# Performance work log

Measured on AMD Instinct MI355X. Metric: run time of the kernel, lower is better.

The kernel has to match this reference:

```python
import jax, jax.numpy as jnp
import numpy as np

D_MODEL = 512
NUM_HEADS = 8
HEAD_DIM = D_MODEL // NUM_HEADS
MAX_REL = 2


def setup_inputs() -> dict:
    key = jax.random.key(0)
    ks = jax.random.split(key, 12)
    B, S = 2, 4096
    std = 1.0 / np.sqrt(D_MODEL)
    inp = {
        'q': jax.random.normal(ks[0], (B, S, D_MODEL), jnp.float32),
        'k': jax.random.normal(ks[1], (B, S, D_MODEL), jnp.float32),
        'v': jax.random.normal(ks[2], (B, S, D_MODEL), jnp.float32),
        'Wq': jax.random.normal(ks[3], (D_MODEL, D_MODEL), jnp.float32) * std,
        'bq': jnp.zeros((D_MODEL,), jnp.float32),
        'Wk': jax.random.normal(ks[4], (D_MODEL, D_MODEL), jnp.float32) * std,
        'bk': jnp.zeros((D_MODEL,), jnp.float32),
        'Wv': jax.random.normal(ks[5], (D_MODEL, D_MODEL), jnp.float32) * std,
        'bv': jnp.zeros((D_MODEL,), jnp.float32),
        'Wo': jax.random.normal(ks[6], (D_MODEL, D_MODEL), jnp.float32) * std,
        'bo': jnp.zeros((D_MODEL,), jnp.float32),
        'rel_pos': jax.random.normal(ks[7], (NUM_HEADS, 2 * MAX_REL + 1), jnp.float32),
    }
    return inp


def _rel_bias(rel_pos, seq_len):
    pos = jnp.arange(seq_len)
    rel = pos[None, :] - pos[:, None]              # [S,S]
    idx = jnp.clip(rel, -MAX_REL, MAX_REL) + MAX_REL
    return rel_pos[:, idx]                         # [H,S,S]


def reference(q, k, v, Wq, bq, Wk, bk, Wv, bv, Wo, bo, rel_pos):
    B, S, D = q.shape
    H, Hd = NUM_HEADS, HEAD_DIM
    # torch Linear: x @ W.T + b
    Q = (q @ Wq.T + bq).reshape(B, S, H, Hd).transpose(0, 2, 1, 3)  # [B,H,S,Hd]
    K = (k @ Wk.T + bk).reshape(B, S, H, Hd).transpose(0, 2, 1, 3)
    V = (v @ Wv.T + bv).reshape(B, S, H, Hd).transpose(0, 2, 1, 3)
    scores = jnp.einsum('bhqd,bhkd->bhqk', Q, K) / jnp.sqrt(jnp.float32(Hd))
    scores = scores + _rel_bias(rel_pos, S)[None]                  # [B,H,S,S]
    probs = jax.nn.softmax(scores, axis=-1)
    attn = jnp.einsum('bhqk,bhkd->bhqd', probs, V)                 # [B,H,S,Hd]
    attn = attn.transpose(0, 2, 1, 3).reshape(B, S, D)
    return attn @ Wo.T + bo
```

## Files before the change

### kernel.cpp

```cpp
#include <hip/hip_runtime.h>

typedef __bf16 bf16_t;
typedef __bf16 bf16x2 __attribute__((ext_vector_type(2)));
typedef __bf16 bf16x4 __attribute__((ext_vector_type(4)));
typedef __bf16 bf16x8 __attribute__((ext_vector_type(8)));
typedef float f32x4 __attribute__((ext_vector_type(4)));
typedef unsigned int u32x4 __attribute__((ext_vector_type(4)));

#define MFMA16(a, b, c) __builtin_amdgcn_mfma_f32_16x16x32_bf16(a, b, c, 0, 0, 0)
#define LOG2E 1.4426950408889634f
#define SHIFT 16.0f

#define GLL(g, l)                                                      \
  __builtin_amdgcn_global_load_lds(                                    \
      (const __attribute__((address_space(1))) void*)(g),              \
      (__attribute__((address_space(3))) void*)(l), 16, 0, 0)

#define WAIT_BARRIER_V0() asm volatile("s_waitcnt vmcnt(0)\n\ts_barrier" ::: "memory")
#define WAIT_BARRIER_V6() asm volatile("s_waitcnt vmcnt(6)\n\ts_barrier" ::: "memory")

static constexpr int NB = 2;
static constexpr int SEQ = 4096;
static constexpr int DM = 512;
static constexpr int NH = 8;
static constexpr int HD = 64;
static constexpr int M_ROWS = NB * SEQ;

__global__ __launch_bounds__(256) void cvt_w_kernel(
    const float* __restrict__ w0, const float* __restrict__ w1,
    const float* __restrict__ w2, const float* __restrict__ w3,
    bf16_t* __restrict__ out) {
  const float* src = (blockIdx.y == 0) ? w0 : (blockIdx.y == 1) ? w1
                   : (blockIdx.y == 2) ? w2 : w3;
  int i = (blockIdx.x * 256 + threadIdx.x) * 4;
  float4 v = *(const float4*)(src + i);
  bf16_t* o = out + blockIdx.y * (DM * DM) + i;
  o[0] = (bf16_t)v.x; o[1] = (bf16_t)v.y; o[2] = (bf16_t)v.z; o[3] = (bf16_t)v.w;
}

__global__ __launch_bounds__(256) void cvt_x_kernel(
    const float* __restrict__ q, const float* __restrict__ k,
    const float* __restrict__ v, bf16_t* __restrict__ out) {
  const float* src = (blockIdx.y == 0) ? q : (blockIdx.y == 1) ? k : v;
  bf16_t* dst = out + (size_t)blockIdx.y * (M_ROWS * DM);
  int i = (blockIdx.x * 256 + threadIdx.x) * 8;
  float4 a = *(const float4*)(src + i);
  float4 b = *(const float4*)(src + i + 4);
  bf16x8 o;
  o[0] = (bf16_t)a.x; o[1] = (bf16_t)a.y; o[2] = (bf16_t)a.z; o[3] = (bf16_t)a.w;
  o[4] = (bf16_t)b.x; o[5] = (bf16_t)b.y; o[6] = (bf16_t)b.z; o[7] = (bf16_t)b.w;
  *(bf16x8*)(dst + i) = o;
}

__device__ __forceinline__ void gemm_body64(
    const bf16_t* __restrict__ X, const bf16_t* __restrict__ Wm,
    const float* __restrict__ bias, void* __restrict__ Out,
    int omode, float scale) {
  __shared__ bf16_t Asm[3][64 * 64];
  __shared__ bf16_t Bsm[3][128 * 64];

  const int tid = threadIdx.x;
  const int w = tid >> 6;
  const int lane = tid & 63;
  const int quad = lane >> 4, l15 = lane & 15;
  const int l8 = lane >> 3;
  const int swcol = ((lane & 7) ^ l8) * 8;
  const int m0 = blockIdx.x * 64;
  const int n0 = blockIdx.y * 128;
  const int moff = (w & 1) * 32;
  const int noff = (w >> 1) * 64;

  f32x4 acc[2][4];
#pragma unroll
  for (int mb = 0; mb < 2; mb++)
#pragma unroll
    for (int nb = 0; nb < 4; nb++) { acc[mb][nb][0] = 0.f; acc[mb][nb][1] = 0.f; acc[mb][nb][2] = 0.f; acc[mb][nb][3] = 0.f; }

  auto stage = [&](int ks, int bufi) {
    const int k0 = ks * 64;
#pragma unroll
    for (int j = 0; j < 4; j++) {
      const int row = j * 32 + w * 8 + l8;
      GLL(Wm + (size_t)(n0 + row) * DM + k0 + swcol, &Bsm[bufi][(j * 256 + w * 64) * 8]);
    }
#pragma unroll
    for (int j = 0; j < 2; j++) {
      const int row = j * 32 + w * 8 + l8;
      GLL(X + (size_t)(m0 + row) * DM + k0 + swcol, &Asm[bufi][(j * 256 + w * 64) * 8]);
    }
  };

  stage(0, 0);
  stage(1, 1);

  for (int ks = 0; ks < 8; ks++) {
    WAIT_BARRIER_V6();
    const int tn = (ks + 2 < 8) ? ks + 2 : 7;
    stage(tn, (ks + 2) % 3);
    const int p = ks % 3;

#pragma unroll
    for (int kd = 0; kd < 2; kd++) {
      const int fch = (((kd << 2) + quad) ^ (l15 & 7)) << 3;
      bf16x8 bfr[4];
#pragma unroll
      for (int nb = 0; nb < 4; nb++)
        bfr[nb] = *(const bf16x8*)&Bsm[p][(noff + nb * 16 + l15) * 64 + fch];
#pragma unroll
      for (int mb = 0; mb < 2; mb++) {
        bf16x8 a = *(const bf16x8*)&Asm[p][(moff + mb * 16 + l15) * 64 + fch];
#pragma unroll
        for (int nb = 0; nb < 4; nb++) acc[mb][nb] = MFMA16(a, bfr[nb], acc[mb][nb]);
      }
    }
  }

#pragma unroll
  for (int nb = 0; nb < 4; nb++) {
    const int n = n0 + noff + nb * 16 + l15;
    const float bn = bias[n];
    const int h = n >> 6, dd = n & 63;
#pragma unroll
    for (int mb = 0; mb < 2; mb++) {
      const int mbase = m0 + moff + mb * 16 + quad * 4;
      const int bb = mbase >> 12, s = mbase & 4095;
      if (omode == 0) {
#pragma unroll
        for (int r = 0; r < 4; r++) {
          const float val = (acc[mb][nb][r] + bn) * scale;
          ((bf16_t*)Out)[(size_t)((bb * NH + h) * SEQ + s + r) * HD + dd] = (bf16_t)val;
        }
      } else if (omode == 1) {
        bf16x4 pk;
#pragma unroll
        for (int r = 0; r < 4; r++) pk[r] = (bf16_t)(acc[mb][nb][r] + bn);
        *(bf16x4*)&((bf16_t*)Out)[(((size_t)(bb * NH + h) * HD + dd) << 12) + s] = pk;
      } else {
#pragma unroll
        for (int r = 0; r < 4; r++)
          ((float*)Out)[(size_t)(mbase + r) * DM + n] = acc[mb][nb][r] + bn;
      }
    }
  }
}

__global__ __launch_bounds__(256, 2) void qkv_kernel(
    const bf16_t* __restrict__ Xall, const bf16_t* __restrict__ Wall,
    const float* __restrict__ bq, const float* __restrict__ bk,
    const float* __restrict__ bv, bf16_t* __restrict__ Qb,
    bf16_t* __restrict__ Kb, bf16_t* __restrict__ Vb, float qscale) {
  const int z = blockIdx.z;
  const bf16_t* X = Xall + (size_t)z * (M_ROWS * DM);
  const float* bias = (z == 0) ? bq : (z == 1) ? bk : bv;
  bf16_t* Out = (z == 0) ? Qb : (z == 1) ? Kb : Vb;
  gemm_body64(X, Wall + (size_t)z * DM * DM, bias, Out,
              (z == 2) ? 1 : 0, (z == 0) ? qscale : 1.0f);
}

__global__ __launch_bounds__(256, 2) void oproj_kernel(
    const bf16_t* __restrict__ X, const bf16_t* __restrict__ Wm,
    const float* __restrict__ bias, float* __restrict__ Out) {
  gemm_body64(X, Wm, bias, Out, 2, 1.0f);
}

__global__ __launch_bounds__(256, 2) void attn_kernel(
    const bf16_t* __restrict__ Qb, const bf16_t* __restrict__ Kb,
    const bf16_t* __restrict__ Vb, const float* __restrict__ rel_pos,
    bf16_t* __restrict__ attn_out) {
  __shared__ bf16_t Kt[4][64 * 64];
  __shared__ bf16_t Vt[4][64 * 64];

  const int tid = threadIdx.x;
  const int w = tid >> 6;
  const int lane = tid & 63;
  const int quad = lane >> 4, l15 = lane & 15;
  const int wq = w >> 1, wk = w & 1;

  const int lin = blockIdx.x;
  const int glob = (lin & 7) * 64 + (lin >> 3);
  const int bh = glob >> 5;
  const int qb = glob & 31;
  const int b = bh >> 3, h = bh & 7;
  const int qlo = qb * 128 + wq * 64;

  const float rb0 = rel_pos[h * 5 + 0] * LOG2E;
  const float rb1 = rel_pos[h * 5 + 1] * LOG2E;
  const float rb2 = rel_pos[h * 5 + 2] * LOG2E;
  const float rb3 = rel_pos[h * 5 + 3] * LOG2E;
  const float rb4 = rel_pos[h * 5 + 4] * LOG2E;

  bf16x8 qf[4][2];
#pragma unroll
  for (int mb = 0; mb < 4; mb++)
#pragma unroll
    for (int kd = 0; kd < 2; kd++)
      qf[mb][kd] = *(const bf16x8*)(Qb + (size_t)(bh * SEQ + qlo + mb * 16 + l15) * HD + kd * 32 + 8 * quad);

  f32x4 o[4][4];
#pragma unroll
  for (int mb = 0; mb < 4; mb++)
#pragma unroll
    for (int db = 0; db < 4; db++) { o[mb][db][0] = 0.f; o[mb][db][1] = 0.f; o[mb][db][2] = 0.f; o[mb][db][3] = 0.f; }
  f32x4 l4[4];
#pragma unroll
  for (int mb = 0; mb < 4; mb++) { l4[mb][0] = 0.f; l4[mb][1] = 0.f; l4[mb][2] = 0.f; l4[mb][3] = 0.f; }

  bf16x8 ones;
#pragma unroll
  for (int i = 0; i < 8; i++) ones[i] = (bf16_t)1.0f;

  const int srow = (w << 4) + (lane >> 3);
  const int scol = (((lane & 7) ^ (lane >> 3)) << 3);
  const bf16_t* kg0 = Kb + ((size_t)(bh * SEQ + srow) << 6) + scol;
  const bf16_t* vg0 = Vb + (((size_t)(bh * HD + srow)) << 12) + scol;
  const int ldst = (w << 10);

  const int sw = l15 & 7;
  const int kfo0 = (l15 << 6) + ((quad ^ sw) << 3);
  const int kfo1 = (l15 << 6) + (((quad + 4) ^ sw) << 3);
  const int vfo = (l15 << 6) + ((((wk << 2) + quad) ^ sw) << 3);
  const int wk2 = wk << 1;

  auto stage = [&](int t, int bufi) {
    GLL(kg0 + ((size_t)t << 12), &Kt[bufi][ldst]);
    GLL(kg0 + ((size_t)t << 12) + (8 << 6), &Kt[bufi][ldst + 512]);
    GLL(vg0 + (t << 6), &Vt[bufi][ldst]);
    GLL(vg0 + (t << 6) + (8 << 12), &Vt[bufi][ldst + 512]);
  };

  auto qk_tile = [&](int tq, f32x4 (&s)[4][2]) {
    const int klo = tq * 64 + wk * 32;
    float cini;
    if (klo >= qlo + 65)        cini = rb4 - SHIFT;
    else if (klo <= qlo - 33)   cini = rb0 - SHIFT;
    else                        cini = -SHIFT;
#pragma unroll
    for (int mb = 0; mb < 4; mb++)
#pragma unroll
      for (int kb = 0; kb < 2; kb++) { s[mb][kb][0] = cini; s[mb][kb][1] = cini; s[mb][kb][2] = cini; s[mb][kb][3] = cini; }
    const int pq = tq & 3;
    __builtin_amdgcn_s_setprio(1);
#pragma unroll
    for (int kb = 0; kb < 2; kb++) {
      bf16x8 kA0 = *(const bf16x8*)&Kt[pq][kfo0 + ((wk2 + kb) << 10)];
      bf16x8 kA1 = *(const bf16x8*)&Kt[pq][kfo1 + ((wk2 + kb) << 10)];
      s[0][kb] = MFMA16(kA0, qf[0][0], s[0][kb]);
      s[0][kb] = MFMA16(kA1, qf[0][1], s[0][kb]);
      s[1][kb] = MFMA16(kA0, qf[1][0], s[1][kb]);
      s[1][kb] = MFMA16(kA1, qf[1][1], s[1][kb]);
      s[2][kb] = MFMA16(kA0, qf[2][0], s[2][kb]);
      s[2][kb] = MFMA16(kA1, qf[2][1], s[2][kb]);
      s[3][kb] = MFMA16(kA0, qf[3][0], s[3][kb]);
      s[3][kb] = MFMA16(kA1, qf[3][1], s[3][kb]);
    }
    __builtin_amdgcn_s_setprio(0);
  };

  auto sm_pv = [&](int t, f32x4 (&s)[4][2]) {
    const int klo = t * 64 + wk * 32;
    const bool nearband = !(klo >= qlo + 65) && !(klo <= qlo - 33);
    if (nearband) {
#pragma unroll
      for (int mb = 0; mb < 4; mb++) {
        const int qg = qlo + mb * 16 + l15;
#pragma unroll
        for (int kb = 0; kb < 2; kb++)
#pragma unroll
          for (int r = 0; r < 4; r++) {
            int dl = klo + kb * 16 + quad * 4 + r - qg;
            float bias = dl <= -2 ? rb0
                       : (dl >= 2 ? rb4
                       : (dl == -1 ? rb1 : (dl == 0 ? rb2 : rb3)));
            s[mb][kb][r] += bias;
          }
      }
    }

    bf16x8 pf[4];
#pragma unroll
    for (int mb = 0; mb < 4; mb++) {
      unsigned int u[2][2];
#pragma unroll
      for (int kb = 0; kb < 2; kb++) {
        bf16x2 p0, p1;
        p0[0] = (bf16_t)__builtin_amdgcn_exp2f(s[mb][kb][0]);
        p0[1] = (bf16_t)__builtin_amdgcn_exp2f(s[mb][kb][1]);
        p1[0] = (bf16_t)__builtin_amdgcn_exp2f(s[mb][kb][2]);
        p1[1] = (bf16_t)__builtin_amdgcn_exp2f(s[mb][kb][3]);
        u[kb][0] = __builtin_bit_cast(unsigned int, p0);
        u[kb][1] = __builtin_bit_cast(unsigned int, p1);
      }
      unsigned int a0 = u[0][0], b0 = u[1][0];
      unsigned int a1 = u[0][1], b1 = u[1][1];
      asm("v_permlane32_swap_b32 %0, %1" : "+v"(a0), "+v"(b0));
      asm("v_permlane32_swap_b32 %0, %1" : "+v"(a1), "+v"(b1));
      asm("v_permlane16_swap_b32 %0, %1" : "+v"(a0), "+v"(b0));
      asm("v_permlane16_swap_b32 %0, %1" : "+v"(a1), "+v"(b1));
      u32x4 pk; pk[0] = a0; pk[1] = a1; pk[2] = b0; pk[3] = b1;
      pf[mb] = __builtin_bit_cast(bf16x8, pk);
    }

    const int p = t & 3;
    __builtin_amdgcn_s_setprio(1);
    l4[0] = MFMA16(ones, pf[0], l4[0]);
    l4[1] = MFMA16(ones, pf[1], l4[1]);
    l4[2] = MFMA16(ones, pf[2], l4[2]);
    l4[3] = MFMA16(ones, pf[3], l4[3]);
#pragma unroll
    for (int db = 0; db < 4; db++) {
      bf16x8 vA = *(const bf16x8*)&Vt[p][vfo + (db << 10)];
      o[0][db] = MFMA16(vA, pf[0], o[0][db]);
      o[1][db] = MFMA16(vA, pf[1], o[1][db]);
      o[2][db] = MFMA16(vA, pf[2], o[2][db]);
      o[3][db] = MFMA16(vA, pf[3], o[3][db]);
    }
    __builtin_amdgcn_s_setprio(0);
  };

  stage(0, 0);
  stage(1, 1);

  f32x4 sA[4][2], sB[4][2];

  for (int j = 0; j < 32; j++) {
    const int e = 2 * j, o2 = 2 * j + 1;
    WAIT_BARRIER_V0();
    const int ta = (e + 2 < 64) ? e + 2 : 63;
    const int tb = (o2 + 2 < 64) ? o2 + 2 : 63;
    stage(ta, (e + 2) & 3);
    stage(tb, (o2 + 2) & 3);
    qk_tile(e, sA);
    qk_tile(o2, sB);
    sm_pv(e, sA);
    sm_pv(o2, sB);
  }

  asm volatile("s_waitcnt vmcnt(0)" ::: "memory");
  __syncthreads();
  float* Ored = (float*)&Kt[0][0];
  float* lred = (float*)&Vt[0][0];
  if (wk) {
#pragma unroll
    for (int mb = 0; mb < 4; mb++) {
      lred[(wq << 6) + (mb << 4) + l15] = l4[mb][0];
#pragma unroll
      for (int db = 0; db < 4; db++) {
        const int ch = ((db << 2) | quad) ^ sw;
        *(f32x4*)&Ored[(wq << 12) + ((mb * 16 + l15) << 6) + (ch << 2)] = o[mb][db];
      }
    }
  }
  __syncthreads();
  if (!wk) {
#pragma unroll
    for (int mb = 0; mb < 4; mb++) {
      float lsum = l4[mb][0] + lred[(wq << 6) + (mb << 4) + l15];
      const float inv = 1.0f / lsum;
      const int qg = qlo + mb * 16 + l15;
#pragma unroll
      for (int db = 0; db < 4; db++) {
        const int ch = ((db << 2) | quad) ^ sw;
        const f32x4 part = *(const f32x4*)&Ored[(wq << 12) + ((mb * 16 + l15) << 6) + (ch << 2)];
        bf16x4 pk;
#pragma unroll
        for (int r = 0; r < 4; r++) pk[r] = (bf16_t)((o[mb][db][r] + part[r]) * inv);
        *(bf16x4*)(attn_out + (size_t)(b * SEQ + qg) * DM + h * HD + db * 16 + quad * 4) = pk;
      }
    }
  }
}

extern "C" void kernel_launch(void* const* d_in, const int* in_sizes, int n_in,
                              void* d_out, int out_size, void* d_ws, size_t ws_size,
                              hipStream_t stream) {
  const float* q   = (const float*)d_in[0];
  const float* k   = (const float*)d_in[1];
  const float* v   = (const float*)d_in[2];
  const float* Wq  = (const float*)d_in[3];
  const float* bq  = (const float*)d_in[4];
  const float* Wk  = (const float*)d_in[5];
  const float* bk  = (const float*)d_in[6];
  const float* Wv  = (const float*)d_in[7];
  const float* bv  = (const float*)d_in[8];
  const float* Wo  = (const float*)d_in[9];
  const float* bo  = (const float*)d_in[10];
  const float* rel = (const float*)d_in[11];

  char* ws = (char*)d_ws;
  bf16_t* Wbf  = (bf16_t*)ws;
  bf16_t* Xb   = (bf16_t*)(ws + (size_t)(2  << 20));
  bf16_t* Qbuf = (bf16_t*)(ws + (size_t)(26 << 20));
  bf16_t* Kbuf = (bf16_t*)(ws + (size_t)(34 << 20));
  bf16_t* Vbuf = (bf16_t*)(ws + (size_t)(42 << 20));
  bf16_t* Abuf = (bf16_t*)(ws + (size_t)(2  << 20));

  cvt_w_kernel<<<dim3(256, 4), 256, 0, stream>>>(Wq, Wk, Wv, Wo, Wbf);
  cvt_x_kernel<<<dim3(2048, 3), 256, 0, stream>>>(q, k, v, Xb);

  const float qscale = LOG2E / 8.0f;
  qkv_kernel<<<dim3(128, 4, 3), 256, 0, stream>>>(
      Xb, Wbf, bq, bk, bv, Qbuf, Kbuf, Vbuf, qscale);

  attn_kernel<<<512, 256, 0, stream>>>(Qbuf, Kbuf, Vbuf, rel, Abuf);

  oproj_kernel<<<dim3(128, 4), 256, 0, stream>>>(Abuf, Wbf + 3 * DM * DM, bo, (float*)d_out);
}
```

Baseline: 227.2 us.

## Halve attention query tile and K/V buffering to raise occupancy

The attention kernel now gives each block 64 queries instead of 128 and each wave 32 query rows instead of 64, and launches 1024 blocks. It cuts the K/V LDS ring from 4 stages to 2, drops the two-tile software pipelining in favour of a simple one-tile-per-iteration loop, and raises launch_bounds to 4 blocks per CU. The goal is more resident waves to hide latency, at the cost of loading each K/V tile for half as many queries (double the K/V traffic) and less prefetch depth. The near-band threshold is tightened to match the smaller query span.

```diff
diff --git a/kernel.cpp b/kernel.cpp
--- a/kernel.cpp
+++ b/kernel.cpp
@@ -163,12 +163,12 @@
   gemm_body64(X, Wm, bias, Out, 2, 1.0f);
 }
 
-__global__ __launch_bounds__(256, 2) void attn_kernel(
+__global__ __launch_bounds__(256, 4) void attn_kernel(
     const bf16_t* __restrict__ Qb, const bf16_t* __restrict__ Kb,
     const bf16_t* __restrict__ Vb, const float* __restrict__ rel_pos,
     bf16_t* __restrict__ attn_out) {
-  __shared__ bf16_t Kt[4][64 * 64];
-  __shared__ bf16_t Vt[4][64 * 64];
+  __shared__ bf16_t Kt[2][64 * 64];
+  __shared__ bf16_t Vt[2][64 * 64];
 
   const int tid = threadIdx.x;
   const int w = tid >> 6;
@@ -177,11 +177,11 @@
   const int wq = w >> 1, wk = w & 1;
 
   const int lin = blockIdx.x;
-  const int glob = (lin & 7) * 64 + (lin >> 3);
-  const int bh = glob >> 5;
-  const int qb = glob & 31;
+  const int glob = (lin & 7) * 128 + (lin >> 3);
+  const int bh = glob >> 6;
+  const int qb = glob & 63;
   const int b = bh >> 3, h = bh & 7;
-  const int qlo = qb * 128 + wq * 64;
+  const int qlo = qb * 64 + wq * 32;
 
   const float rb0 = rel_pos[h * 5 + 0] * LOG2E;
   const float rb1 = rel_pos[h * 5 + 1] * LOG2E;
@@ -189,21 +189,21 @@
   const float rb3 = rel_pos[h * 5 + 3] * LOG2E;
   const float rb4 = rel_pos[h * 5 + 4] * LOG2E;
 
-  bf16x8 qf[4][2];
-#pragma unroll
-  for (int mb = 0; mb < 4; mb++)
+  bf16x8 qf[2][2];
+#pragma unroll
+  for (int mb = 0; mb < 2; mb++)
 #pragma unroll
     for (int kd = 0; kd < 2; kd++)
       qf[mb][kd] = *(const bf16x8*)(Qb + (size_t)(bh * SEQ + qlo + mb * 16 + l15) * HD + kd * 32 + 8 * quad);
 
-  f32x4 o[4][4];
-#pragma unroll
-  for (int mb = 0; mb < 4; mb++)
+  f32x4 o[2][4];
+#pragma unroll
+  for (int mb = 0; mb < 2; mb++)
 #pragma unroll
     for (int db = 0; db < 4; db++) { o[mb][db][0] = 0.f; o[mb][db][1] = 0.f; o[mb][db][2] = 0.f; o[mb][db][3] = 0.f; }
-  f32x4 l4[4];
-#pragma unroll
-  for (int mb = 0; mb < 4; mb++) { l4[mb][0] = 0.f; l4[mb][1] = 0.f; l4[mb][2] = 0.f; l4[mb][3] = 0.f; }
+  f32x4 l4[2];
+  l4[0][0] = 0.f; l4[0][1] = 0.f; l4[0][2] = 0.f; l4[0][3] = 0.f;
+  l4[1][0] = 0.f; l4[1][1] = 0.f; l4[1][2] = 0.f; l4[1][3] = 0.f;
 
   bf16x8 ones;
 #pragma unroll
@@ -228,40 +228,40 @@
     GLL(vg0 + (t << 6) + (8 << 12), &Vt[bufi][ldst + 512]);
   };
 
-  auto qk_tile = [&](int tq, f32x4 (&s)[4][2]) {
-    const int klo = tq * 64 + wk * 32;
+  stage(0, 0);
+
+  for (int t = 0; t < 64; t++) {
+    WAIT_BARRIER_V0();
+    if (t + 1 < 64) stage(t + 1, (t + 1) & 1);
+    const int p = t & 1;
+    const int klo = t * 64 + wk * 32;
+
     float cini;
-    if (klo >= qlo + 65)        cini = rb4 - SHIFT;
+    bool nearband = false;
+    if (klo >= qlo + 33)        cini = rb4 - SHIFT;
     else if (klo <= qlo - 33)   cini = rb0 - SHIFT;
-    else                        cini = -SHIFT;
-#pragma unroll
-    for (int mb = 0; mb < 4; mb++)
+    else                        { cini = -SHIFT; nearband = true; }
+
+    f32x4 s[2][2];
+#pragma unroll
+    for (int mb = 0; mb < 2; mb++)
 #pragma unroll
       for (int kb = 0; kb < 2; kb++) { s[mb][kb][0] = cini; s[mb][kb][1] = cini; s[mb][kb][2] = cini; s[mb][kb][3] = cini; }
-    const int pq = tq & 3;
     __builtin_amdgcn_s_setprio(1);
 #pragma unroll
     for (int kb = 0; kb < 2; kb++) {
-      bf16x8 kA0 = *(const bf16x8*)&Kt[pq][kfo0 + ((wk2 + kb) << 10)];
-      bf16x8 kA1 = *(const bf16x8*)&Kt[pq][kfo1 + ((wk2 + kb) << 10)];
+      bf16x8 kA0 = *(const bf16x8*)&Kt[p][kfo0 + ((wk2 + kb) << 10)];
+      bf16x8 kA1 = *(const bf16x8*)&Kt[p][kfo1 + ((wk2 + kb) << 10)];
       s[0][kb] = MFMA16(kA0, qf[0][0], s[0][kb]);
       s[0][kb] = MFMA16(kA1, qf[0][1], s[0][kb]);
       s[1][kb] = MFMA16(kA0, qf[1][0], s[1][kb]);
       s[1][kb] = MFMA16(kA1, qf[1][1], s[1][kb]);
-      s[2][kb] = MFMA16(kA0, qf[2][0], s[2][kb]);
-      s[2][kb] = MFMA16(kA1, qf[2][1], s[2][kb]);
-      s[3][kb] = MFMA16(kA0, qf[3][0], s[3][kb]);
-      s[3][kb] = MFMA16(kA1, qf[3][1], s[3][kb]);
     }
     __builtin_amdgcn_s_setprio(0);
-  };
-
-  auto sm_pv = [&](int t, f32x4 (&s)[4][2]) {
-    const int klo = t * 64 + wk * 32;
-    const bool nearband = !(klo >= qlo + 65) && !(klo <= qlo - 33);
+
     if (nearband) {
 #pragma unroll
-      for (int mb = 0; mb < 4; mb++) {
+      for (int mb = 0; mb < 2; mb++) {
         const int qg = qlo + mb * 16 + l15;
 #pragma unroll
         for (int kb = 0; kb < 2; kb++)
@@ -276,9 +276,9 @@
       }
     }
 
-    bf16x8 pf[4];
-#pragma unroll
-    for (int mb = 0; mb < 4; mb++) {
+    bf16x8 pf[2];
+#pragma unroll
+    for (int mb = 0; mb < 2; mb++) {
       unsigned int u[2][2];
 #pragma unroll
       for (int kb = 0; kb < 2; kb++) {
@@ -300,39 +300,16 @@
       pf[mb] = __builtin_bit_cast(bf16x8, pk);
     }
 
-    const int p = t & 3;
     __builtin_amdgcn_s_setprio(1);
     l4[0] = MFMA16(ones, pf[0], l4[0]);
     l4[1] = MFMA16(ones, pf[1], l4[1]);
-    l4[2] = MFMA16(ones, pf[2], l4[2]);
-    l4[3] = MFMA16(ones, pf[3], l4[3]);
 #pragma unroll
     for (int db = 0; db < 4; db++) {
       bf16x8 vA = *(const bf16x8*)&Vt[p][vfo + (db << 10)];
       o[0][db] = MFMA16(vA, pf[0], o[0][db]);
       o[1][db] = MFMA16(vA, pf[1], o[1][db]);
-      o[2][db] = MFMA16(vA, pf[2], o[2][db]);
-      o[3][db] = MFMA16(vA, pf[3], o[3][db]);
     }
     __builtin_amdgcn_s_setprio(0);
-  };
-
-  stage(0, 0);
-  stage(1, 1);
-
-  f32x4 sA[4][2], sB[4][2];
-
-  for (int j = 0; j < 32; j++) {
-    const int e = 2 * j, o2 = 2 * j + 1;
-    WAIT_BARRIER_V0();
-    const int ta = (e + 2 < 64) ? e + 2 : 63;
-    const int tb = (o2 + 2 < 64) ? o2 + 2 : 63;
-    stage(ta, (e + 2) & 3);
-    stage(tb, (o2 + 2) & 3);
-    qk_tile(e, sA);
-    qk_tile(o2, sB);
-    sm_pv(e, sA);
-    sm_pv(o2, sB);
   }
 
   asm volatile("s_waitcnt vmcnt(0)" ::: "memory");
@@ -341,26 +318,26 @@
   float* lred = (float*)&Vt[0][0];
   if (wk) {
 #pragma unroll
-    for (int mb = 0; mb < 4; mb++) {
-      lred[(wq << 6) + (mb << 4) + l15] = l4[mb][0];
+    for (int mb = 0; mb < 2; mb++) {
+      lred[(wq << 5) + (mb << 4) + l15] = l4[mb][0];
 #pragma unroll
       for (int db = 0; db < 4; db++) {
         const int ch = ((db << 2) | quad) ^ sw;
-        *(f32x4*)&Ored[(wq << 12) + ((mb * 16 + l15) << 6) + (ch << 2)] = o[mb][db];
+        *(f32x4*)&Ored[(wq << 11) + ((mb * 16 + l15) << 6) + (ch << 2)] = o[mb][db];
       }
     }
   }
   __syncthreads();
   if (!wk) {
 #pragma unroll
-    for (int mb = 0; mb < 4; mb++) {
-      float lsum = l4[mb][0] + lred[(wq << 6) + (mb << 4) + l15];
+    for (int mb = 0; mb < 2; mb++) {
+      float lsum = l4[mb][0] + lred[(wq << 5) + (mb << 4) + l15];
       const float inv = 1.0f / lsum;
       const int qg = qlo + mb * 16 + l15;
 #pragma unroll
       for (int db = 0; db < 4; db++) {
         const int ch = ((db << 2) | quad) ^ sw;
-        const f32x4 part = *(const f32x4*)&Ored[(wq << 12) + ((mb * 16 + l15) << 6) + (ch << 2)];
+        const f32x4 part = *(const f32x4*)&Ored[(wq << 11) + ((mb * 16 + l15) << 6) + (ch << 2)];
         bf16x4 pk;
 #pragma unroll
         for (int r = 0; r < 4; r++) pk[r] = (bf16_t)((o[mb][db][r] + part[r]) * inv);
@@ -401,7 +378,7 @@
   qkv_kernel<<<dim3(128, 4, 3), 256, 0, stream>>>(
       Xb, Wbf, bq, bk, bv, Qbuf, Kbuf, Vbuf, qscale);
 
-  attn_kernel<<<512, 256, 0, stream>>>(Qbuf, Kbuf, Vbuf, rel, Abuf);
+  attn_kernel<<<1024, 256, 0, stream>>>(Qbuf, Kbuf, Vbuf, rel, Abuf);
 
   oproj_kernel<<<dim3(128, 4), 256, 0, stream>>>(Abuf, Wbf + 3 * DM * DM, bo, (float*)d_out);
 }
```

Result: slower. 233.9 us (+3.0%).
